# Optimization experiments

Measured on AMD Instinct MI355X. Metric: run time of the kernel, lower is better.

The kernel has to match this reference:

```python
import jax, jax.numpy as jnp
import numpy as np

E, B, D, T = 8, 4096, 2048, 2048
H = D // 2 + T // 2  # expert hidden dim = 2048
TOP_K = 2


def setup_inputs() -> dict:
    key = jax.random.key(0)
    ks = jax.random.split(key, 5)
    s_in = 1.0 / np.sqrt(D)
    s_h = 1.0 / np.sqrt(H)
    return {
        "xs": jax.random.normal(ks[0], (E, B, D), dtype=jnp.float32),
        "Wg": jax.random.normal(ks[1], (D,), dtype=jnp.float32) * s_in,
        "bg": jnp.zeros((1,), dtype=jnp.float32),
        "W1": jax.random.normal(ks[2], (E, D, H), dtype=jnp.float32) * s_in,
        "b1": jnp.zeros((E, H), dtype=jnp.float32),
        "W2": jax.random.normal(ks[3], (E, H, T), dtype=jnp.float32) * s_h,
        "b2": jnp.zeros((E, T), dtype=jnp.float32),
    }


def reference(xs, Wg, bg, W1, b1, W2, b2):
    # Gating: logits[b, e] = x[e][b] @ Wg + bg  -> [B, E]
    logits = jnp.einsum("ebd,d->be", xs, Wg) + bg
    probs = jax.nn.softmax(logits, axis=1)
    top_k_values, top_k_indices = jax.lax.top_k(probs, TOP_K)  # [B, K]

    # Dense expert compute over each expert's own input stream.
    # hidden[e, b, h] = relu(x[e] @ W1[e] + b1[e]); out[e, b, t] = hidden @ W2[e] + b2[e]
    hidden = jax.nn.relu(jnp.einsum("ebd,edh->ebh", xs, W1) + b1[:, None, :])
    expert_out = jnp.einsum("ebh,eht->ebt", hidden, W2) + b2[:, None, :]  # [E, B, T]

    # Gather the top-k experts per token. In the original, masked-dense compute
    # + output mask is mathematically identical to this gather.
    per_token = jnp.transpose(expert_out, (1, 0, 2))  # [B, E, T]
    selected = jnp.take_along_axis(per_token, top_k_indices[:, :, None], axis=1)  # [B, K, T]

    out = jnp.sum(top_k_values[:, :, None] * selected, axis=1)  # [B, T]
    return out, top_k_values
```

## Files before the change

### kernel.cpp

```cpp
#include <hip/hip_runtime.h>
#include <hip/hip_bf16.h>
#include <stdint.h>

#define E_ 8
#define B_ 4096
#define D_ 2048
#define T_ 2048
#define H_ 2048
#define KDIM 2048
#define NDIM 2048

typedef __attribute__((ext_vector_type(4))) float f32x4;
typedef __attribute__((ext_vector_type(4))) unsigned short u16x4;
typedef __attribute__((ext_vector_type(8))) unsigned short u16x8;
typedef __attribute__((ext_vector_type(8))) __bf16 bf16x8;

__device__ __forceinline__ unsigned short f2bf(float f) {
    __hip_bfloat16 h = __float2bfloat16(f);
    return __builtin_bit_cast(unsigned short, h);
}

__device__ __forceinline__ void gload_lds16(const void* g, void* lds) {
    __builtin_amdgcn_global_load_lds(
        (const __attribute__((address_space(1))) void*)g,
        (__attribute__((address_space(3))) void*)lds, 16, 0, 0);
}

__global__ __launch_bounds__(256) void moe_gating(
    const float* __restrict__ xs, const float* __restrict__ Wg,
    const float* __restrict__ bg, float* __restrict__ out_topk,
    float* __restrict__ prob_slot, int* __restrict__ counts,
    int* __restrict__ slot_of, unsigned short* __restrict__ A1)
{
    const int b = blockIdx.x;
    const int t = threadIdx.x;
    const int wave = t >> 6, lane = t & 63;
    __shared__ float red[E_][4];
    __shared__ int sh_i0, sh_i1;

    const f32x4 wg0 = ((const f32x4*)Wg)[t];
    const f32x4 wg1 = ((const f32x4*)Wg)[t + 256];

    f32x4 xa[E_], xb[E_];
    #pragma unroll
    for (int e = 0; e < E_; ++e) {
        const f32x4* xr = (const f32x4*)(xs + ((size_t)e * B_ + b) * D_);
        xa[e] = __builtin_nontemporal_load(&xr[t]);
        xb[e] = __builtin_nontemporal_load(&xr[t + 256]);
        float p = xa[e].x*wg0.x + xa[e].y*wg0.y + xa[e].z*wg0.z + xa[e].w*wg0.w
                + xb[e].x*wg1.x + xb[e].y*wg1.y + xb[e].z*wg1.z + xb[e].w*wg1.w;
        #pragma unroll
        for (int off = 32; off >= 1; off >>= 1) p += __shfl_xor(p, off);
        if (lane == 0) red[e][wave] = p;
    }
    __syncthreads();
    if (t == 0) {
        float pr[E_];
        float mx = -3.0e38f;
        #pragma unroll
        for (int e = 0; e < E_; ++e) {
            pr[e] = red[e][0] + red[e][1] + red[e][2] + red[e][3] + bg[0];
            mx = fmaxf(mx, pr[e]);
        }
        float s = 0.f;
        #pragma unroll
        for (int e = 0; e < E_; ++e) { pr[e] = expf(pr[e] - mx); s += pr[e]; }
        float inv = 1.0f / s;
        #pragma unroll
        for (int e = 0; e < E_; ++e) pr[e] *= inv;
        int i0 = 0;
        #pragma unroll
        for (int e = 1; e < E_; ++e) if (pr[e] > pr[i0]) i0 = e;
        int i1 = (i0 == 0) ? 1 : 0;
        #pragma unroll
        for (int e = 0; e < E_; ++e) { if (e != i0 && pr[e] > pr[i1]) i1 = e; }
        float p0 = pr[i0], p1 = pr[i1];
        out_topk[2*b]    = p0;
        out_topk[2*b+1]  = p1;
        prob_slot[2*b]   = p0;
        prob_slot[2*b+1] = p1;
        int pos0 = atomicAdd(&counts[i0], 1);
        slot_of[i0 * B_ + pos0] = 2*b;
        int pos1 = atomicAdd(&counts[i1], 1);
        slot_of[i1 * B_ + pos1] = 2*b + 1;
        sh_i0 = i0; sh_i1 = i1;
    }
    __syncthreads();
    const int i0 = sh_i0, i1 = sh_i1;
    f32x4 s0a = xa[0], s0b = xb[0], s1a = xa[0], s1b = xb[0];
    #pragma unroll
    for (int e = 0; e < E_; ++e) {
        if (i0 == e) { s0a = xa[e]; s0b = xb[e]; }
        if (i1 == e) { s1a = xa[e]; s1b = xb[e]; }
    }
    u16x4 w;
    w[0]=f2bf(s0a.x); w[1]=f2bf(s0a.y); w[2]=f2bf(s0a.z); w[3]=f2bf(s0a.w);
    ((u16x4*)(A1 + (size_t)(2*b) * D_))[t] = w;
    w[0]=f2bf(s0b.x); w[1]=f2bf(s0b.y); w[2]=f2bf(s0b.z); w[3]=f2bf(s0b.w);
    ((u16x4*)(A1 + (size_t)(2*b) * D_ + 1024))[t] = w;
    w[0]=f2bf(s1a.x); w[1]=f2bf(s1a.y); w[2]=f2bf(s1a.z); w[3]=f2bf(s1a.w);
    ((u16x4*)(A1 + (size_t)(2*b+1) * D_))[t] = w;
    w[0]=f2bf(s1b.x); w[1]=f2bf(s1b.y); w[2]=f2bf(s1b.z); w[3]=f2bf(s1b.w);
    ((u16x4*)(A1 + (size_t)(2*b+1) * D_ + 1024))[t] = w;
}

__global__ void build_tiles(const int* __restrict__ counts, int* __restrict__ tiles)
{
    if (threadIdx.x == 0 && blockIdx.x == 0) {
        int n = 0;
        for (int e = 0; e < E_; ++e) {
            int te = (counts[e] + 255) >> 8;
            for (int m = 0; m < te; ++m) tiles[1 + n++] = (e << 16) | m;
        }
        tiles[0] = n;
    }
}

__global__ __launch_bounds__(256) void wtrans(
    const float* __restrict__ W, unsigned short* __restrict__ Wt)
{
    const int e  = blockIdx.z;
    const int kb = blockIdx.x * 64;
    const int nb = blockIdx.y * 64;
    const int t  = threadIdx.x;
    __shared__ float tile[64][68];

    const float* src = W + ((size_t)e * KDIM + kb) * NDIM + nb;
    {
        const int kr = t >> 2, nc = (t & 3) * 16;
        #pragma unroll
        for (int j = 0; j < 4; ++j) {
            f32x4 v = __builtin_nontemporal_load(
                (const f32x4*)(src + (size_t)kr * NDIM + nc + j * 4));
            *(f32x4*)&tile[kr][nc + j * 4] = v;
        }
    }
    __syncthreads();
    {
        const int nn = t >> 2, kc = (t & 3) * 16;
        unsigned short wbuf[16];
        #pragma unroll
        for (int j = 0; j < 16; ++j) wbuf[j] = f2bf(tile[kc + j][nn]);
        unsigned short* dst = Wt + ((size_t)e * NDIM + nb + nn) * KDIM + kb + kc;
        *(u16x8*)dst       = *(const u16x8*)&wbuf[0];
        *((u16x8*)dst + 1) = *(const u16x8*)&wbuf[8];
    }
}

#define BAR  __builtin_amdgcn_s_barrier()

template<int LAYER>
__global__ __launch_bounds__(1024, 4) void moe_gemm(
    const unsigned short* __restrict__ Abuf,
    const unsigned short* __restrict__ Wt,
    const float* __restrict__ bias,
    const int* __restrict__ counts,
    const int* __restrict__ tiles,
    const int* __restrict__ slot_of,
    const float* __restrict__ prob_slot,
    unsigned short* __restrict__ hidden_out,
    float* __restrict__ out)
{
    const int nMt = tiles[0];
    const int bid = blockIdx.x;
    const int mt  = bid >> 3;
    const int np  = bid & 7;
    if (mt >= nMt) return;
    const int info = tiles[1 + mt];
    const int e   = info >> 16;
    const int m0  = (info & 0xffff) * 256;
    const int n0  = np * 256;
    const int n_e = counts[e];

    const int t = threadIdx.x;
    const int lane = t & 63;
    const int w = t >> 6;
    const int wm = (w >> 2) * 64;
    const int wn = (w & 3) * 64;
    const int lg = lane >> 4;

    __shared__ u16x8 As[4 * 1024];
    __shared__ u16x8 Bs[4 * 1024];
    __shared__ int   slots_s[256];
    __shared__ float probs_s[256];

    if (t < 256) {
        int gm = m0 + t;
        int s = -1; float p = 0.f;
        if (gm < n_e) { s = slot_of[e * B_ + gm]; p = prob_slot[s]; }
        slots_s[t] = s; probs_s[t] = p;
    }
    __syncthreads();

    const int ksw = (((t & 3) ^ ((t >> 3) & 3)) << 3);
    const unsigned short* aptr;
    const unsigned short* bptr;
    {
        const int r = t >> 2;
        int s = slots_s[r]; if (s < 0) s = 0;
        aptr = Abuf + (size_t)s * KDIM + ksw;
        bptr = Wt + ((size_t)e * NDIM + n0 + r) * KDIM + ksw;
    }

#define STG(BUF, KT) do{ \
    gload_lds16(aptr + (KT)*32, &As[(BUF)*1024 + w*64]); \
    gload_lds16(bptr + (KT)*32, &Bs[(BUF)*1024 + w*64]); }while(0)

    f32x4 acc[4][4];
    #pragma unroll
    for (int i = 0; i < 4; ++i)
        #pragma unroll
        for (int j = 0; j < 4; ++j) {
            f32x4 z = {0.f, 0.f, 0.f, 0.f};
            acc[i][j] = z;
        }

    STG(0, 0); STG(1, 1); STG(2, 2);

    const int usw = (lane >> 1) & 3;
    for (int kt = 0; kt < 64; ++kt) {
        asm volatile("s_waitcnt vmcnt(4)" ::: "memory");
        BAR;
        int tn = kt + 3; if (tn > 63) tn = 63;
        STG((kt + 3) & 3, tn);

        const int base = (kt & 3) * 1024;
        bf16x8 af[4];
        #pragma unroll
        for (int mi = 0; mi < 4; ++mi) {
            const int row = wm + mi * 16 + (lane & 15);
            af[mi] = __builtin_bit_cast(bf16x8, As[base + row * 4 + (lg ^ usw)]);
        }
        #pragma unroll
        for (int ni = 0; ni < 4; ++ni) {
            const int row = wn + ni * 16 + (lane & 15);
            bf16x8 bq = __builtin_bit_cast(bf16x8, Bs[base + row * 4 + (lg ^ usw)]);
            #pragma unroll
            for (int mi = 0; mi < 4; ++mi)
                acc[mi][ni] = __builtin_amdgcn_mfma_f32_16x16x32_bf16(
                    af[mi], bq, acc[mi][ni], 0, 0, 0);
        }
    }
    asm volatile("s_waitcnt vmcnt(0)" ::: "memory");

    #pragma unroll
    for (int mi = 0; mi < 4; ++mi) {
        #pragma unroll
        for (int rr = 0; rr < 4; ++rr) {
            const int rloc = wm + mi * 16 + ((lane >> 4) << 2) + rr;
            const int s = slots_s[rloc];
            if (s < 0) continue;
            #pragma unroll
            for (int ni = 0; ni < 4; ++ni) {
                const int col = n0 + wn + ni * 16 + (lane & 15);
                float v = acc[mi][ni][rr];
                if (LAYER == 1) {
                    v += bias[e * NDIM + col];
                    v = fmaxf(v, 0.f);
                    hidden_out[(size_t)s * H_ + col] = f2bf(v);
                } else {
                    v = (v + bias[e * NDIM + col]) * probs_s[rloc];
                    atomicAdd(&out[(size_t)(s >> 1) * T_ + col], v);
                }
            }
        }
    }
#undef STG
}

extern "C" void kernel_launch(void* const* d_in, const int* in_sizes, int n_in,
                              void* d_out, int out_size, void* d_ws, size_t ws_size,
                              hipStream_t stream)
{
    const float* xs = (const float*)d_in[0];
    const float* Wg = (const float*)d_in[1];
    const float* bg = (const float*)d_in[2];
    const float* W1 = (const float*)d_in[3];
    const float* b1 = (const float*)d_in[4];
    const float* W2 = (const float*)d_in[5];
    const float* b2 = (const float*)d_in[6];

    float* out      = (float*)d_out;
    float* out_topk = out + (size_t)B_ * T_;

    char* ws = (char*)d_ws;
    int*   counts    = (int*)ws;
    int*   tiles     = (int*)(ws + 256);
    int*   slot_of   = (int*)(ws + 768);
    float* prob_slot = (float*)(ws + 768 + E_ * B_ * 4);
    size_t off = 768 + (size_t)E_ * B_ * 4 + 2 * B_ * 4;
    off = (off + 255) & ~(size_t)255;
    unsigned short* A1     = (unsigned short*)(ws + off); off += (size_t)2 * B_ * D_ * 2;
    unsigned short* hidden = (unsigned short*)(ws + off); off += (size_t)2 * B_ * H_ * 2;
    unsigned short* Wtb    = (unsigned short*)(ws + off);

    hipMemsetAsync(counts, 0, 256, stream);
    hipMemsetAsync(out, 0, (size_t)B_ * T_ * sizeof(float), stream);

    dim3 tgrid(32, 32, E_), blk(256);
    dim3 ggrid(39 * 8);
    dim3 gblk(1024);

    moe_gating<<<dim3(B_), dim3(256), 0, stream>>>(
        xs, Wg, bg, out_topk, prob_slot, counts, slot_of, A1);
    build_tiles<<<dim3(1), dim3(64), 0, stream>>>(counts, tiles);

    wtrans<<<tgrid, blk, 0, stream>>>(W1, Wtb);
    moe_gemm<1><<<ggrid, gblk, 0, stream>>>(
        A1, Wtb, b1, counts, tiles, slot_of, prob_slot, hidden, nullptr);

    wtrans<<<tgrid, blk, 0, stream>>>(W2, Wtb);
    moe_gemm<2><<<ggrid, gblk, 0, stream>>>(
        hidden, Wtb, b2, counts, tiles, slot_of, prob_slot, nullptr, out);
}
```

Before: 527.9 us.

## Merge weight transposes into one launch and interleave GEMM loads with MFMA priority

```diff
diff --git a/kernel.cpp b/kernel.cpp
--- a/kernel.cpp
+++ b/kernel.cpp
@@ -116,10 +116,15 @@
     }
 }
 
+template<int DUAL>
 __global__ __launch_bounds__(256) void wtrans(
-    const float* __restrict__ W, unsigned short* __restrict__ Wt)
-{
-    const int e  = blockIdx.z;
+    const float* __restrict__ Wa, const float* __restrict__ Wb,
+    unsigned short* __restrict__ Wta, unsigned short* __restrict__ Wtb)
+{
+    const int z  = blockIdx.z;
+    const int e  = DUAL ? (z & 7) : z;
+    const float* W = (DUAL && (z >> 3)) ? Wb : Wa;
+    unsigned short* Wt = (DUAL && (z >> 3)) ? Wtb : Wta;
     const int kb = blockIdx.x * 64;
     const int nb = blockIdx.y * 64;
     const int t  = threadIdx.x;
@@ -148,6 +153,8 @@
 }
 
 #define BAR  __builtin_amdgcn_s_barrier()
+#define PRIO1 __builtin_amdgcn_s_setprio(1)
+#define PRIO0 __builtin_amdgcn_s_setprio(0)
 
 template<int LAYER>
 __global__ __launch_bounds__(1024, 4) void moe_gemm(
@@ -202,9 +209,8 @@
         bptr = Wt + ((size_t)e * NDIM + n0 + r) * KDIM + ksw;
     }
 
-#define STG(BUF, KT) do{ \
-    gload_lds16(aptr + (KT)*32, &As[(BUF)*1024 + w*64]); \
-    gload_lds16(bptr + (KT)*32, &Bs[(BUF)*1024 + w*64]); }while(0)
+#define STGA(BUF, KT) gload_lds16(aptr + (KT)*32, &As[(BUF)*1024 + w*64])
+#define STGB(BUF, KT) gload_lds16(bptr + (KT)*32, &Bs[(BUF)*1024 + w*64])
 
     f32x4 acc[4][4];
     #pragma unroll
@@ -215,31 +221,57 @@
             acc[i][j] = z;
         }
 
-    STG(0, 0); STG(1, 1); STG(2, 2);
+    STGA(0, 0); STGB(0, 0);
+    STGA(1, 1); STGB(1, 1);
+    STGA(2, 2); STGB(2, 2);
 
     const int usw = (lane >> 1) & 3;
     for (int kt = 0; kt < 64; ++kt) {
         asm volatile("s_waitcnt vmcnt(4)" ::: "memory");
         BAR;
         int tn = kt + 3; if (tn > 63) tn = 63;
-        STG((kt + 3) & 3, tn);
-
+        const int nb = (kt + 3) & 3;
         const int base = (kt & 3) * 1024;
+
+        STGA(nb, tn);
         bf16x8 af[4];
         #pragma unroll
         for (int mi = 0; mi < 4; ++mi) {
             const int row = wm + mi * 16 + (lane & 15);
             af[mi] = __builtin_bit_cast(bf16x8, As[base + row * 4 + (lg ^ usw)]);
         }
-        #pragma unroll
-        for (int ni = 0; ni < 4; ++ni) {
-            const int row = wn + ni * 16 + (lane & 15);
-            bf16x8 bq = __builtin_bit_cast(bf16x8, Bs[base + row * 4 + (lg ^ usw)]);
-            #pragma unroll
-            for (int mi = 0; mi < 4; ++mi)
-                acc[mi][ni] = __builtin_amdgcn_mfma_f32_16x16x32_bf16(
-                    af[mi], bq, acc[mi][ni], 0, 0, 0);
-        }
+        bf16x8 bq0, bq1;
+        {
+            const int r0 = wn + 0 * 16 + (lane & 15);
+            const int r1 = wn + 1 * 16 + (lane & 15);
+            bq0 = __builtin_bit_cast(bf16x8, Bs[base + r0 * 4 + (lg ^ usw)]);
+            bq1 = __builtin_bit_cast(bf16x8, Bs[base + r1 * 4 + (lg ^ usw)]);
+        }
+        PRIO1;
+        #pragma unroll
+        for (int mi = 0; mi < 4; ++mi)
+            acc[mi][0] = __builtin_amdgcn_mfma_f32_16x16x32_bf16(af[mi], bq0, acc[mi][0], 0, 0, 0);
+        #pragma unroll
+        for (int mi = 0; mi < 4; ++mi)
+            acc[mi][1] = __builtin_amdgcn_mfma_f32_16x16x32_bf16(af[mi], bq1, acc[mi][1], 0, 0, 0);
+        PRIO0;
+
+        STGB(nb, tn);
+        bf16x8 bq2, bq3;
+        {
+            const int r2 = wn + 2 * 16 + (lane & 15);
+            const int r3 = wn + 3 * 16 + (lane & 15);
+            bq2 = __builtin_bit_cast(bf16x8, Bs[base + r2 * 4 + (lg ^ usw)]);
+            bq3 = __builtin_bit_cast(bf16x8, Bs[base + r3 * 4 + (lg ^ usw)]);
+        }
+        PRIO1;
+        #pragma unroll
+        for (int mi = 0; mi < 4; ++mi)
+            acc[mi][2] = __builtin_amdgcn_mfma_f32_16x16x32_bf16(af[mi], bq2, acc[mi][2], 0, 0, 0);
+        #pragma unroll
+        for (int mi = 0; mi < 4; ++mi)
+            acc[mi][3] = __builtin_amdgcn_mfma_f32_16x16x32_bf16(af[mi], bq3, acc[mi][3], 0, 0, 0);
+        PRIO0;
     }
     asm volatile("s_waitcnt vmcnt(0)" ::: "memory");
 
@@ -265,7 +297,8 @@
             }
         }
     }
-#undef STG
+#undef STGA
+#undef STGB
 }
 
 extern "C" void kernel_launch(void* const* d_in, const int* in_sizes, int n_in,
@@ -292,24 +325,38 @@
     off = (off + 255) & ~(size_t)255;
     unsigned short* A1     = (unsigned short*)(ws + off); off += (size_t)2 * B_ * D_ * 2;
     unsigned short* hidden = (unsigned short*)(ws + off); off += (size_t)2 * B_ * H_ * 2;
-    unsigned short* Wtb    = (unsigned short*)(ws + off);
+    unsigned short* Wt1    = (unsigned short*)(ws + off); off += (size_t)E_ * KDIM * NDIM * 2;
+    size_t off_big = off + (size_t)E_ * KDIM * NDIM * 2;
+    unsigned short* Wt2 = (unsigned short*)(ws + off);
+
+    const bool big = (ws_size >= off_big);
 
     hipMemsetAsync(counts, 0, 256, stream);
     hipMemsetAsync(out, 0, (size_t)B_ * T_ * sizeof(float), stream);
 
-    dim3 tgrid(32, 32, E_), blk(256);
+    dim3 blk(256), gblk(1024);
     dim3 ggrid(39 * 8);
-    dim3 gblk(1024);
-
-    moe_gating<<<dim3(B_), dim3(256), 0, stream>>>(
-        xs, Wg, bg, out_topk, prob_slot, counts, slot_of, A1);
-    build_tiles<<<dim3(1), dim3(64), 0, stream>>>(counts, tiles);
-
-    wtrans<<<tgrid, blk, 0, stream>>>(W1, Wtb);
-    moe_gemm<1><<<ggrid, gblk, 0, stream>>>(
-        A1, Wtb, b1, counts, tiles, slot_of, prob_slot, hidden, nullptr);
-
-    wtrans<<<tgrid, blk, 0, stream>>>(W2, Wtb);
-    moe_gemm<2><<<ggrid, gblk, 0, stream>>>(
-        hidden, Wtb, b2, counts, tiles, slot_of, prob_slot, nullptr, out);
-}
+
+    if (big) {
+        dim3 tgrid(32, 32, 16);
+        wtrans<1><<<tgrid, blk, 0, stream>>>(W1, W2, Wt1, Wt2);
+        moe_gating<<<dim3(B_), dim3(256), 0, stream>>>(
+            xs, Wg, bg, out_topk, prob_slot, counts, slot_of, A1);
+        build_tiles<<<dim3(1), dim3(64), 0, stream>>>(counts, tiles);
+        moe_gemm<1><<<ggrid, gblk, 0, stream>>>(
+            A1, Wt1, b1, counts, tiles, slot_of, prob_slot, hidden, nullptr);
+        moe_gemm<2><<<ggrid, gblk, 0, stream>>>(
+            hidden, Wt2, b2, counts, tiles, slot_of, prob_slot, nullptr, out);
+    } else {
+        dim3 tgrid(32, 32, E_);
+        moe_gating<<<dim3(B_), dim3(256), 0, stream>>>(
+            xs, Wg, bg, out_topk, prob_slot, counts, slot_of, A1);
+        build_tiles<<<dim3(1), dim3(64), 0, stream>>>(counts, tiles);
+        wtrans<0><<<tgrid, blk, 0, stream>>>(W1, nullptr, Wt1, nullptr);
+        moe_gemm<1><<<ggrid, gblk, 0, stream>>>(
+            A1, Wt1, b1, counts, tiles, slot_of, prob_slot, hidden, nullptr);
+        wtrans<0><<<tgrid, blk, 0, stream>>>(W2, nullptr, Wt1, nullptr);
+        moe_gemm<2><<<ggrid, gblk, 0, stream>>>(
+            hidden, Wt1, b2, counts, tiles, slot_of, prob_slot, nullptr, out);
+    }
+}
```

Measured after the change: 528.1 us. Within noise of the previous version (+0.0%).
